# Kernel optimization log

Hardware: AMD Instinct MI355X
Metric: run time of the kernel (lower is better)

The kernel has to match this reference:

```python
import jax, jax.numpy as jnp
import numpy as np

H = 150  # hidden size
STEPS = 10


def setup_inputs() -> dict:
    key = jax.random.key(0)
    ks = jax.random.split(key, 5)
    inputx = jax.random.normal(ks[0], (16, 1, H), dtype=jnp.float32)
    W_ih = jax.random.normal(ks[1], (4 * H, H), dtype=jnp.float32) * (1.0 / np.sqrt(H))
    W_hh = jax.random.normal(ks[2], (4 * H, H), dtype=jnp.float32) * (1.0 / np.sqrt(H))
    b_ih = jax.random.normal(ks[3], (4 * H,), dtype=jnp.float32) * (1.0 / np.sqrt(H))
    b_hh = jax.random.normal(ks[4], (4 * H,), dtype=jnp.float32) * (1.0 / np.sqrt(H))
    return {"inputx": inputx, "W_ih": W_ih, "W_hh": W_hh, "b_ih": b_ih, "b_hh": b_hh, "x": 13}


def _lstm_forward(inputx, W_ih, W_hh, b_ih, b_hh, x):
    # xs: the 10 steps inputx[x-10], ..., inputx[x-1], each [1, H]
    xs = inputx[x - STEPS:x]
    h0 = jnp.zeros((1, H), dtype=inputx.dtype)
    c0 = jnp.zeros((1, H), dtype=inputx.dtype)

    def step(carry, xt):
        h, c = carry
        # PyTorch LSTMCell: gates in order (i, f, g, o)
        gates = xt @ W_ih.T + b_ih + h @ W_hh.T + b_hh  # [1, 4H]
        i_g, f_g, g_g, o_g = jnp.split(gates, 4, axis=-1)
        c_new = jax.nn.sigmoid(f_g) * c + jax.nn.sigmoid(i_g) * jnp.tanh(g_g)
        h_new = jax.nn.sigmoid(o_g) * jnp.tanh(c_new)
        return (h_new, c_new), None

    (h_t, _), _ = jax.lax.scan(step, (h0, c0), xs)
    return h_t  # [1, H]


def reference(inputx, W_ih, W_hh, b_ih, b_hh, x):
    return _lstm_forward(inputx, W_ih, W_hh, b_ih, b_hh, x)
```

## Files before the change

### kernel.cpp

```cpp
#include <hip/hip_runtime.h>
#include <hip/hip_fp16.h>
#include <math.h>

#define H 150
#define G 600
#define STEPS 10
#define NT 320
#define WPR 76
#define NPK (WPR * G)
#define NGXB 19
#define NPKB 109
#define NPREP (NGXB + NPKB)
#define GXW 16
#define MAGIC 0x13579BDFu

#define GXP_WORDS (G * GXW)
#define SLOT_OFF (GXP_WORDS + NPK)

typedef _Float16 half2v __attribute__((ext_vector_type(2)));

__device__ __forceinline__ float sigm(float x) {
    return __builtin_amdgcn_rcpf(1.0f + __expf(-x));
}
__device__ __forceinline__ float ftanh(float x) {
    return 1.0f - 2.0f * __builtin_amdgcn_rcpf(1.0f + __expf(2.0f * x));
}
__device__ __forceinline__ float dot2(float acc, unsigned w, unsigned h) {
#if __has_builtin(__builtin_amdgcn_fdot2)
    return __builtin_amdgcn_fdot2(__builtin_bit_cast(half2v, w),
                                  __builtin_bit_cast(half2v, h), acc, false);
#else
    half2v wv = __builtin_bit_cast(half2v, w);
    half2v hv = __builtin_bit_cast(half2v, h);
    return acc + (float)wv.x * (float)hv.x + (float)wv.y * (float)hv.y;
#endif
}
__device__ __forceinline__ unsigned short f2h(float x) {
    _Float16 h = (_Float16)x;
    return __builtin_bit_cast(unsigned short, h);
}

__global__ __launch_bounds__(NT) void lstm_all(
    const float* __restrict__ inputx, const float* __restrict__ W_ih,
    const float* __restrict__ W_hh, const float* __restrict__ b_ih,
    const float* __restrict__ b_hh, const int* __restrict__ xp,
    float* __restrict__ gxp, unsigned* __restrict__ Wp,
    unsigned* __restrict__ slots, float* __restrict__ out)
{
    const int tid = threadIdx.x;
    const int blk = blockIdx.x;

    if (blk > 0) {
        const int p = blk - 1;
        if (p < NGXB) {
            int gid = p * NT + tid;
            if (gid < STEPS * G) {
                int g  = gid / STEPS;
                int st = gid - g * STEPS;
                const float* xrow = inputx + (xp[0] - STEPS + st) * H;
                const float* wrow = W_ih + g * H;
                float a0 = 0.f, a1 = 0.f;
                #pragma unroll
                for (int k = 0; k < H; k += 2) {
                    float2 wv = *reinterpret_cast<const float2*>(wrow + k);
                    float2 xv = *reinterpret_cast<const float2*>(xrow + k);
                    a0 += wv.x * xv.x;
                    a1 += wv.y * xv.y;
                }
                gxp[g * GXW + st] = a0 + a1 + b_ih[g] + b_hh[g];
            }
        } else {
            for (int i = (p - NGXB) * NT + tid; i < NPK; i += NPKB * NT) {
                int jh = i / 2400;
                int r  = i - jh * 2400;
                int g  = r >> 2;
                int j  = 4 * jh + (r & 3);
                unsigned v = 0;
                if (j < 75) {
                    const float* row = W_hh + g * H + 2 * j;
                    v = ((unsigned)f2h(row[1]) << 16) | (unsigned)f2h(row[0]);
                }
                Wp[i] = v;
            }
        }
        __syncthreads();
        if (tid == 0) {
            __threadfence();
            atomicExch(&slots[p], MAGIC);
        }
        return;
    }

    __shared__ __align__(16) unsigned short s_hh[2 * WPR];
    __shared__ float s_gate[G];

    if (tid < NPREP) {
        while (atomicAdd(&slots[tid], 0u) != MAGIC) __builtin_amdgcn_s_sleep(2);
    }
    __threadfence();
    __syncthreads();

    const bool rowt = (tid < 300);
    const bool actt = (tid < H);

    unsigned w[2 * WPR];
    if (rowt) {
        const uint4* W4 = reinterpret_cast<const uint4*>(Wp);
        #pragma unroll
        for (int jh = 0; jh < 19; ++jh) {
            uint4 v = W4[jh * 600 + tid];
            w[4 * jh] = v.x; w[4 * jh + 1] = v.y;
            w[4 * jh + 2] = v.z; w[4 * jh + 3] = v.w;
        }
        #pragma unroll
        for (int jh = 0; jh < 19; ++jh) {
            uint4 v = W4[jh * 600 + 300 + tid];
            w[WPR + 4 * jh] = v.x; w[WPR + 4 * jh + 1] = v.y;
            w[WPR + 4 * jh + 2] = v.z; w[WPR + 4 * jh + 3] = v.w;
        }
    }
    float gxr0[STEPS], gxr1[STEPS];
    if (rowt) {
        const float* r0 = gxp + tid * GXW;
        const float* r1 = gxp + (300 + tid) * GXW;
        float4 q0 = *reinterpret_cast<const float4*>(r0);
        float4 q1 = *reinterpret_cast<const float4*>(r0 + 4);
        float2 q2 = *reinterpret_cast<const float2*>(r0 + 8);
        gxr0[0]=q0.x; gxr0[1]=q0.y; gxr0[2]=q0.z; gxr0[3]=q0.w;
        gxr0[4]=q1.x; gxr0[5]=q1.y; gxr0[6]=q1.z; gxr0[7]=q1.w;
        gxr0[8]=q2.x; gxr0[9]=q2.y;
        float4 p0 = *reinterpret_cast<const float4*>(r1);
        float4 p1 = *reinterpret_cast<const float4*>(r1 + 4);
        float2 p2 = *reinterpret_cast<const float2*>(r1 + 8);
        gxr1[0]=p0.x; gxr1[1]=p0.y; gxr1[2]=p0.z; gxr1[3]=p0.w;
        gxr1[4]=p1.x; gxr1[5]=p1.y; gxr1[6]=p1.z; gxr1[7]=p1.w;
        gxr1[8]=p2.x; gxr1[9]=p2.y;
    }

    if (tid < 2 * WPR) s_hh[tid] = 0;
    float c = 0.f;
    float hlast = 0.f;
    __syncthreads();

    #pragma unroll 1
    for (int st = 0; st < STEPS; ++st) {
        if (rowt) {
            float a0 = 0.f, a1 = 0.f, a2 = 0.f, a3 = 0.f;
            float b0 = 0.f, b1 = 0.f, b2 = 0.f, b3 = 0.f;
            #pragma unroll
            for (int cc = 0; cc < 19; ++cc) {
                float4 hv = *reinterpret_cast<const float4*>(
                    reinterpret_cast<const char*>(s_hh) + 16 * cc);
                unsigned h0 = __float_as_uint(hv.x);
                unsigned h1 = __float_as_uint(hv.y);
                unsigned h2 = __float_as_uint(hv.z);
                unsigned h3 = __float_as_uint(hv.w);
                a0 = dot2(a0, w[4 * cc],     h0);
                a1 = dot2(a1, w[4 * cc + 1], h1);
                a2 = dot2(a2, w[4 * cc + 2], h2);
                a3 = dot2(a3, w[4 * cc + 3], h3);
                b0 = dot2(b0, w[WPR + 4 * cc],     h0);
                b1 = dot2(b1, w[WPR + 4 * cc + 1], h1);
                b2 = dot2(b2, w[WPR + 4 * cc + 2], h2);
                b3 = dot2(b3, w[WPR + 4 * cc + 3], h3);
            }
            s_gate[tid]       = gxr0[st] + (a0 + a1) + (a2 + a3);
            s_gate[300 + tid] = gxr1[st] + (b0 + b1) + (b2 + b3);
        }
        __syncthreads();
        if (actt) {
            float ig = s_gate[tid];
            float fg = s_gate[H + tid];
            float gg = s_gate[2 * H + tid];
            float og = s_gate[3 * H + tid];
            float cn = sigm(fg) * c + sigm(ig) * ftanh(gg);
            float hn = sigm(og) * ftanh(cn);
            c = cn;
            hlast = hn;
            s_hh[tid] = f2h(hn);
        }
        __syncthreads();
    }

    if (actt) out[tid] = hlast;
}

__global__ __launch_bounds__(640) void lstm_fused(
    const float* __restrict__ inputx, const float* __restrict__ W_ih,
    const float* __restrict__ W_hh, const float* __restrict__ b_ih,
    const float* __restrict__ b_hh, const int* __restrict__ xp,
    float* __restrict__ out)
{
    __shared__ float s_h[H];
    __shared__ float s_c[H];
    __shared__ float s_gate[G];
    __shared__ float s_x[STEPS * H];

    const int tid = threadIdx.x;
    if (tid < H) { s_h[tid] = 0.f; s_c[tid] = 0.f; }
    const int x0 = (xp[0] - STEPS) * H;
    for (int i = tid; i < STEPS * H; i += 640) s_x[i] = inputx[x0 + i];
    __syncthreads();

    for (int t = 0; t < STEPS; ++t) {
        if (tid < G) {
            const float* wi = W_ih + tid * H;
            const float* wh = W_hh + tid * H;
            float acc = b_ih[tid] + b_hh[tid];
            for (int k = 0; k < H; ++k)
                acc += wi[k] * s_x[t * H + k] + wh[k] * s_h[k];
            s_gate[tid] = acc;
        }
        __syncthreads();
        if (tid < H) {
            float ig = s_gate[tid], fg = s_gate[H + tid];
            float gg = s_gate[2 * H + tid], og = s_gate[3 * H + tid];
            float cn = sigm(fg) * s_c[tid] + sigm(ig) * ftanh(gg);
            s_c[tid] = cn;
            s_h[tid] = sigm(og) * ftanh(cn);
        }
        __syncthreads();
    }
    if (tid < H) out[tid] = s_h[tid];
}

extern "C" void kernel_launch(void* const* d_in, const int* in_sizes, int n_in,
                              void* d_out, int out_size, void* d_ws, size_t ws_size,
                              hipStream_t stream) {
    const float* inputx = (const float*)d_in[0];
    const float* W_ih   = (const float*)d_in[1];
    const float* W_hh   = (const float*)d_in[2];
    const float* b_ih   = (const float*)d_in[3];
    const float* b_hh   = (const float*)d_in[4];
    const int*   xp     = (const int*)d_in[5];
    float* out = (float*)d_out;

    const size_t need = (size_t)(SLOT_OFF + NPREP) * sizeof(unsigned);
    if (ws_size >= need) {
        float*    gxp   = (float*)d_ws;
        unsigned* Wp    = (unsigned*)d_ws + GXP_WORDS;
        unsigned* slots = (unsigned*)d_ws + SLOT_OFF;
        lstm_all<<<NPREP + 1, NT, 0, stream>>>(inputx, W_ih, W_hh, b_ih, b_hh,
                                               xp, gxp, Wp, slots, out);
    } else {
        lstm_fused<<<1, 640, 0, stream>>>(inputx, W_ih, W_hh, b_ih, b_hh, xp, out);
    }
}
```

Before: 20.66 us.

## Load weights speculatively before flag wait and split gate activations across thread halves

The main block now loads packed weights and input-gate preactivations before checking the producer flags. It checks all flags once with a block-wide AND, and only spins and reloads if some were not yet set. Row assignment is remapped so threads 0-149 own the i/f gates and threads 150-299 own g/o. Each half applies its own sigmoid/tanh directly, so only one float2 per unit goes through shared memory instead of the full gate array. This cuts activation work per thread and drops the final barrier. The speculative load may read stale data and then has to be repeated.

```diff
diff --git a/kernel.cpp b/kernel.cpp
--- a/kernel.cpp
+++ b/kernel.cpp
@@ -47,13 +47,13 @@
     float* __restrict__ gxp, unsigned* __restrict__ Wp,
     unsigned* __restrict__ slots, float* __restrict__ out)
 {
-    const int tid = threadIdx.x;
+    const int t   = threadIdx.x;
     const int blk = blockIdx.x;
 
     if (blk > 0) {
         const int p = blk - 1;
         if (p < NGXB) {
-            int gid = p * NT + tid;
+            int gid = p * NT + t;
             if (gid < STEPS * G) {
                 int g  = gid / STEPS;
                 int st = gid - g * STEPS;
@@ -70,7 +70,7 @@
                 gxp[g * GXW + st] = a0 + a1 + b_ih[g] + b_hh[g];
             }
         } else {
-            for (int i = (p - NGXB) * NT + tid; i < NPK; i += NPKB * NT) {
+            for (int i = (p - NGXB) * NT + t; i < NPK; i += NPKB * NT) {
                 int jh = i / 2400;
                 int r  = i - jh * 2400;
                 int g  = r >> 2;
@@ -84,7 +84,7 @@
             }
         }
         __syncthreads();
-        if (tid == 0) {
+        if (t == 0) {
             __threadfence();
             atomicExch(&slots[p], MAGIC);
         }
@@ -92,59 +92,68 @@
     }
 
     __shared__ __align__(16) unsigned short s_hh[2 * WPR];
-    __shared__ float s_gate[G];
-
-    if (tid < NPREP) {
-        while (atomicAdd(&slots[tid], 0u) != MAGIC) __builtin_amdgcn_s_sleep(2);
-    }
-    __threadfence();
-    __syncthreads();
-
-    const bool rowt = (tid < 300);
-    const bool actt = (tid < H);
+    __shared__ float2 s_ex[H];
+
+    const bool work = (t < 300);
+    const int r0 = (t < 150) ? t : t + 150;
+    const int r1 = r0 + 150;
 
     unsigned w[2 * WPR];
-    if (rowt) {
-        const uint4* W4 = reinterpret_cast<const uint4*>(Wp);
-        #pragma unroll
-        for (int jh = 0; jh < 19; ++jh) {
-            uint4 v = W4[jh * 600 + tid];
-            w[4 * jh] = v.x; w[4 * jh + 1] = v.y;
-            w[4 * jh + 2] = v.z; w[4 * jh + 3] = v.w;
-        }
-        #pragma unroll
-        for (int jh = 0; jh < 19; ++jh) {
-            uint4 v = W4[jh * 600 + 300 + tid];
-            w[WPR + 4 * jh] = v.x; w[WPR + 4 * jh + 1] = v.y;
-            w[WPR + 4 * jh + 2] = v.z; w[WPR + 4 * jh + 3] = v.w;
-        }
-    }
-    float gxr0[STEPS], gxr1[STEPS];
-    if (rowt) {
-        const float* r0 = gxp + tid * GXW;
-        const float* r1 = gxp + (300 + tid) * GXW;
-        float4 q0 = *reinterpret_cast<const float4*>(r0);
-        float4 q1 = *reinterpret_cast<const float4*>(r0 + 4);
-        float2 q2 = *reinterpret_cast<const float2*>(r0 + 8);
-        gxr0[0]=q0.x; gxr0[1]=q0.y; gxr0[2]=q0.z; gxr0[3]=q0.w;
-        gxr0[4]=q1.x; gxr0[5]=q1.y; gxr0[6]=q1.z; gxr0[7]=q1.w;
-        gxr0[8]=q2.x; gxr0[9]=q2.y;
-        float4 p0 = *reinterpret_cast<const float4*>(r1);
-        float4 p1 = *reinterpret_cast<const float4*>(r1 + 4);
-        float2 p2 = *reinterpret_cast<const float2*>(r1 + 8);
-        gxr1[0]=p0.x; gxr1[1]=p0.y; gxr1[2]=p0.z; gxr1[3]=p0.w;
-        gxr1[4]=p1.x; gxr1[5]=p1.y; gxr1[6]=p1.z; gxr1[7]=p1.w;
-        gxr1[8]=p2.x; gxr1[9]=p2.y;
-    }
-
-    if (tid < 2 * WPR) s_hh[tid] = 0;
+    float gx0[STEPS], gx1[STEPS];
+
+    auto load_all = [&]() {
+        if (work) {
+            const uint4* W4 = reinterpret_cast<const uint4*>(Wp);
+            #pragma unroll
+            for (int jh = 0; jh < 19; ++jh) {
+                uint4 v = W4[jh * 600 + r0];
+                w[4 * jh] = v.x; w[4 * jh + 1] = v.y;
+                w[4 * jh + 2] = v.z; w[4 * jh + 3] = v.w;
+            }
+            #pragma unroll
+            for (int jh = 0; jh < 19; ++jh) {
+                uint4 v = W4[jh * 600 + r1];
+                w[WPR + 4 * jh] = v.x; w[WPR + 4 * jh + 1] = v.y;
+                w[WPR + 4 * jh + 2] = v.z; w[WPR + 4 * jh + 3] = v.w;
+            }
+            const float* ra = gxp + r0 * GXW;
+            const float* rb = gxp + r1 * GXW;
+            float4 q0 = *reinterpret_cast<const float4*>(ra);
+            float4 q1 = *reinterpret_cast<const float4*>(ra + 4);
+            float2 q2 = *reinterpret_cast<const float2*>(ra + 8);
+            gx0[0]=q0.x; gx0[1]=q0.y; gx0[2]=q0.z; gx0[3]=q0.w;
+            gx0[4]=q1.x; gx0[5]=q1.y; gx0[6]=q1.z; gx0[7]=q1.w;
+            gx0[8]=q2.x; gx0[9]=q2.y;
+            float4 p0 = *reinterpret_cast<const float4*>(rb);
+            float4 p1 = *reinterpret_cast<const float4*>(rb + 4);
+            float2 p2 = *reinterpret_cast<const float2*>(rb + 8);
+            gx1[0]=p0.x; gx1[1]=p0.y; gx1[2]=p0.z; gx1[3]=p0.w;
+            gx1[4]=p1.x; gx1[5]=p1.y; gx1[6]=p1.z; gx1[7]=p1.w;
+            gx1[8]=p2.x; gx1[9]=p2.y;
+        }
+    };
+
+    load_all();
+    if (t < 2 * WPR) s_hh[t] = 0;
+
+    int ok = 1;
+    if (t < NPREP) ok = (atomicAdd(&slots[t], 0u) == MAGIC) ? 1 : 0;
+    if (__syncthreads_and(ok) == 0) {
+        if (t < NPREP) {
+            while (atomicAdd(&slots[t], 0u) != MAGIC) __builtin_amdgcn_s_sleep(2);
+        }
+        __syncthreads();
+        __threadfence();
+        load_all();
+        __syncthreads();
+    }
+
     float c = 0.f;
-    float hlast = 0.f;
-    __syncthreads();
+    float si = 0.f, sf = 0.f;
 
     #pragma unroll 1
     for (int st = 0; st < STEPS; ++st) {
-        if (rowt) {
+        if (work) {
             float a0 = 0.f, a1 = 0.f, a2 = 0.f, a3 = 0.f;
             float b0 = 0.f, b1 = 0.f, b2 = 0.f, b3 = 0.f;
             #pragma unroll
@@ -164,25 +173,25 @@
                 b2 = dot2(b2, w[WPR + 4 * cc + 2], h2);
                 b3 = dot2(b3, w[WPR + 4 * cc + 3], h3);
             }
-            s_gate[tid]       = gxr0[st] + (a0 + a1) + (a2 + a3);
-            s_gate[300 + tid] = gxr1[st] + (b0 + b1) + (b2 + b3);
-        }
-        __syncthreads();
-        if (actt) {
-            float ig = s_gate[tid];
-            float fg = s_gate[H + tid];
-            float gg = s_gate[2 * H + tid];
-            float og = s_gate[3 * H + tid];
-            float cn = sigm(fg) * c + sigm(ig) * ftanh(gg);
-            float hn = sigm(og) * ftanh(cn);
-            c = cn;
-            hlast = hn;
-            s_hh[tid] = f2h(hn);
-        }
-        __syncthreads();
-    }
-
-    if (actt) out[tid] = hlast;
+            float d0 = gx0[st] + (a0 + a1) + (a2 + a3);
+            float d1 = gx1[st] + (b0 + b1) + (b2 + b3);
+            if (t < 150) {
+                si = sigm(d0);
+                sf = sigm(d1);
+            } else {
+                s_ex[t - 150] = make_float2(ftanh(d0), sigm(d1));
+            }
+        }
+        __syncthreads();
+        if (t < 150) {
+            float2 ex = s_ex[t];
+            c = sf * c + si * ex.x;
+            float h = ex.y * ftanh(c);
+            if (st == STEPS - 1) out[t] = h;
+            else                 s_hh[t] = f2h(h);
+        }
+        if (st < STEPS - 1) __syncthreads();
+    }
 }
 
 __global__ __launch_bounds__(640) void lstm_fused(
```

Measured after the change: 19.81 us. 1.04x faster.
